# Kernel tuning notes

Hardware: AMD Instinct MI355X
Metric: run time of the kernel (lower is better)

Reference implementation:

```python
import jax, jax.numpy as jnp
import numpy as np

B, S, D, H, NL, FE = 2, 1024, 1024, 16, 6, 4
HD = D // H
DFF = D * FE
EPS = 1e-5


def setup_inputs() -> dict:
    key = jax.random.key(0)
    ks = jax.random.split(key, 12)
    sd = 0.02
    n = lambda k, sh: (jax.random.normal(k, sh, jnp.float32) * sd)
    return {
        "x": jax.random.normal(ks[0], (B, S, D), jnp.float32),
        "pos": n(ks[1], (1, S, D)),
        "Wq": n(ks[2], (NL, HD, HD)), "bq": jnp.zeros((NL, HD), jnp.float32),
        "Wk": n(ks[3], (NL, HD, HD)), "bk": jnp.zeros((NL, HD), jnp.float32),
        "Wv": n(ks[4], (NL, HD, HD)), "bv": jnp.zeros((NL, HD), jnp.float32),
        "Wfc": n(ks[5], (NL, D, D)), "bfc": jnp.zeros((NL, D), jnp.float32),
        "ln1_w": jnp.ones((NL, D), jnp.float32), "ln1_b": jnp.zeros((NL, D), jnp.float32),
        "ln2_w": jnp.ones((NL, D), jnp.float32), "ln2_b": jnp.zeros((NL, D), jnp.float32),
        "W1": n(ks[6], (NL, D, DFF)), "b1": jnp.zeros((NL, DFF), jnp.float32),
        "W2": n(ks[7], (NL, DFF, D)), "b2": jnp.zeros((NL, D), jnp.float32),
        "lnf_w": jnp.ones((D,), jnp.float32), "lnf_b": jnp.zeros((D,), jnp.float32),
    }


def _ln(z, w, b):
    m = jnp.mean(z, axis=-1, keepdims=True)
    v = jnp.mean(jnp.square(z - m), axis=-1, keepdims=True)
    return (z - m) * jax.lax.rsqrt(v + EPS) * w + b


def reference(x, pos, Wq, bq, Wk, bk, Wv, bv, Wfc, bfc,
              ln1_w, ln1_b, ln2_w, ln2_b, W1, b1, W2, b2, lnf_w, lnf_b):
    Bx, Sx, Dx = x.shape
    causal = jnp.tril(jnp.ones((Sx, Sx), bool))  # [S,S], broadcast over b,h
    y = x + pos[:, :Sx, :]
    scale = 1.0 / jnp.sqrt(jnp.float32(HD))
    for i in range(NL):
        yh = y.reshape(Bx, Sx, H, HD)
        # per-head Linear with weights SHARED across heads (as in source)
        q = yh @ Wq[i] + bq[i]
        k = yh @ Wk[i] + bk[i]
        v = yh @ Wv[i] + bv[i]
        score = jnp.einsum("bqhd,bkhd->bhqk", q, k)
        # masked_fill(-1e20) BEFORE scaling, as in source
        score = jnp.where(causal, score, jnp.float32(-1e20)) * scale
        attn = jax.nn.softmax(score, axis=-1)
        o = jnp.einsum("bhqk,bkhd->bqhd", attn, v).reshape(Bx, Sx, D)
        o = o @ Wfc[i] + bfc[i]
        add = _ln(o + y, ln1_w[i], ln1_b[i])
        ff = jax.nn.gelu(add @ W1[i] + b1[i], approximate=False) @ W2[i] + b2[i]
        y = _ln(ff + add, ln2_w[i], ln2_b[i])
    return _ln(y, lnf_w, lnf_b)
```

## Files before the change

kernel.cpp:

```cpp
#include <hip/hip_runtime.h>
#include <hip/hip_bf16.h>
#include <math.h>

#define B_   2
#define S_   1024
#define D_   1024
#define H_   16
#define HD_  64
#define NL_  6
#define DFF_ 4096

typedef __bf16 bf16_t;
typedef bf16_t bf16x8 __attribute__((ext_vector_type(8)));
typedef bf16_t bf16x4 __attribute__((ext_vector_type(4)));
typedef float  f32x4  __attribute__((ext_vector_type(4)));

__device__ __forceinline__ float gelu_exact(float x) {
    return 0.5f * x * (1.0f + erff(x * 0.70710678118654752f));
}

__device__ __forceinline__ void gload16(const bf16_t* g, bf16_t* l) {
    __builtin_amdgcn_global_load_lds(
        (const __attribute__((address_space(1))) void*)g,
        (__attribute__((address_space(3))) void*)l, 16, 0, 0);
}

__global__ __launch_bounds__(256) void add_pos_kernel(
    const float* __restrict__ x, const float* __restrict__ pos,
    float* __restrict__ y, bf16_t* __restrict__ yb)
{
    int idx = blockIdx.x * 256 + threadIdx.x;
    f32x4 xv = *(const f32x4*)&x[idx * 4];
    f32x4 pv = *(const f32x4*)&pos[(idx & 262143) * 4];
    f32x4 o = xv + pv;
    *(f32x4*)&y[idx * 4] = o;
    *(bf16x4*)&yb[idx * 4] = __builtin_convertvector(o, bf16x4);
}

__global__ __launch_bounds__(256) void qkv_mfma_kernel(
    const bf16_t* __restrict__ yb,
    const float* __restrict__ Wq, const float* __restrict__ bq,
    const float* __restrict__ Wk, const float* __restrict__ bk,
    const float* __restrict__ Wv, const float* __restrict__ bv,
    bf16_t* __restrict__ q, bf16_t* __restrict__ k, bf16_t* __restrict__ v)
{
    __shared__ __align__(16) bf16_t As[128][72];
    __shared__ __align__(16) bf16_t Wt[3][64][72];

    int tid = threadIdx.x;
    long m0 = (long)blockIdx.x * 128;

#pragma unroll
    for (int it = 0; it < 4; ++it) {
        int c = it * 256 + tid;
        int row = c >> 3, col = (c & 7) * 8;
        *(bf16x8*)&As[row][col] = *(const bf16x8*)&yb[(m0 + row) * 64 + col];
    }
#pragma unroll
    for (int it = 0; it < 16; ++it) {
        int i = it * 256 + tid;
        int r = i >> 6, c = i & 63;
        Wt[0][c][r] = (bf16_t)Wq[i];
        Wt[1][c][r] = (bf16_t)Wk[i];
        Wt[2][c][r] = (bf16_t)Wv[i];
    }
    __syncthreads();

    int wave = tid >> 6, lane = tid & 63;
    int quad = lane >> 4, l16 = lane & 15;
    int wm = wave * 32;

    bf16x8 a[2][2];
#pragma unroll
    for (int i = 0; i < 2; ++i)
#pragma unroll
        for (int ks = 0; ks < 2; ++ks)
            a[i][ks] = *(bf16x8*)&As[wm + i * 16 + l16][ks * 32 + quad * 8];

    f32x4 acc[3][2][4];
#pragma unroll
    for (int o = 0; o < 3; ++o)
#pragma unroll
        for (int i = 0; i < 2; ++i)
#pragma unroll
            for (int j = 0; j < 4; ++j) acc[o][i][j] = (f32x4)0.f;

#pragma unroll
    for (int o = 0; o < 3; ++o)
#pragma unroll
        for (int j = 0; j < 4; ++j) {
            bf16x8 b0 = *(bf16x8*)&Wt[o][j * 16 + l16][quad * 8];
            bf16x8 b1 = *(bf16x8*)&Wt[o][j * 16 + l16][32 + quad * 8];
#pragma unroll
            for (int i = 0; i < 2; ++i) {
                acc[o][i][j] = __builtin_amdgcn_mfma_f32_16x16x32_bf16(a[i][0], b0, acc[o][i][j], 0, 0, 0);
                acc[o][i][j] = __builtin_amdgcn_mfma_f32_16x16x32_bf16(a[i][1], b1, acc[o][i][j], 0, 0, 0);
            }
        }

    bf16_t* outs[3] = { q, k, v };
    const float* biases[3] = { bq, bk, bv };
#pragma unroll
    for (int o = 0; o < 3; ++o)
#pragma unroll
        for (int j = 0; j < 4; ++j) {
            int col = j * 16 + l16;
            float bias = biases[o][col];
#pragma unroll
            for (int i = 0; i < 2; ++i) {
                long rbase = m0 + wm + i * 16 + quad * 4;
#pragma unroll
                for (int r = 0; r < 4; ++r)
                    outs[o][(rbase + r) * 64 + col] = (bf16_t)(acc[o][i][j][r] + bias);
            }
        }
}

__global__ __launch_bounds__(256) void vtrans_kernel(
    const bf16_t* __restrict__ vb, bf16_t* __restrict__ vT)
{
    __shared__ __align__(16) bf16_t L[32][72];
    int tid = threadIdx.x;
    int s0 = blockIdx.x * 32;
    int bh = blockIdx.y;
    int b = bh >> 4, h = bh & 15;
    int sr = tid >> 3, dc = (tid & 7) * 8;
    *(bf16x8*)&L[sr][dc] =
        *(const bf16x8*)&vb[(((long)b * S_ + s0 + sr) * H_ + h) * HD_ + dc];
    __syncthreads();
    int dr = tid >> 2, sg = (tid & 3) * 8;
    bf16x8 o;
#pragma unroll
    for (int j = 0; j < 8; ++j) o[j] = L[sg + j][dr];
    *(bf16x8*)&vT[((long)bh * HD_ + dr) * S_ + s0 + sg] = o;
}

__global__ __launch_bounds__(256) void attn_mfma_kernel(
    const bf16_t* __restrict__ Q, const bf16_t* __restrict__ K,
    const bf16_t* __restrict__ VT, bf16_t* __restrict__ Ob)
{
    __shared__ __align__(16) bf16_t Ks[64][72];
    __shared__ __align__(16) bf16_t Vt[64][72];
    __shared__ __align__(16) bf16_t Ps[4][16][72];

    int tid = threadIdx.x;
    int wave = tid >> 6, lane = tid & 63;
    int quad = lane >> 4, l16 = lane & 15;
    int qidx = (blockIdx.x < 8) ? (int)blockIdx.x : 23 - (int)blockIdx.x;
    int q0 = qidx * 64;
    int bh = blockIdx.y;
    int b = bh >> 4, h = bh & 15;
    int qw = q0 + wave * 16;
    const float scale = 0.125f;
    const float MASKED = -1.25e19f;

    const bf16_t* Qbase = Q + (((long)b * S_ + qw + l16) * H_ + h) * HD_;
    bf16x8 aq0 = *(const bf16x8*)&Qbase[quad * 8];
    bf16x8 aq1 = *(const bf16x8*)&Qbase[32 + quad * 8];

    float mrun = -3.0e38f, lrun = 0.f;
    f32x4 oacc[4];
#pragma unroll
    for (int n = 0; n < 4; ++n) oacc[n] = (f32x4)0.f;

    int srow = tid >> 3, scol = (tid & 7) * 8;
    const bf16_t* VTbase = VT + ((long)bh * HD_ ) * S_;
    int qg = qw + l16;

    int nkt = qidx + 1;
    for (int kt = 0; kt < nkt; ++kt) {
        int k0 = kt * 64;
        __syncthreads();
#pragma unroll
        for (int half = 0; half < 2; ++half) {
            int row = half * 32 + srow;
            *(bf16x8*)&Ks[row][scol] =
                *(const bf16x8*)&K[(((long)b * S_ + k0 + row) * H_ + h) * HD_ + scol];
            *(bf16x8*)&Vt[row][scol] =
                *(const bf16x8*)&VTbase[(long)row * S_ + k0 + scol];
        }
        __syncthreads();

        if (k0 > qw + 15) continue;

        f32x4 sc[4];
#pragma unroll
        for (int n = 0; n < 4; ++n) sc[n] = (f32x4)0.f;
#pragma unroll
        for (int n = 0; n < 4; ++n) {
            bf16x8 ak0 = *(bf16x8*)&Ks[n * 16 + l16][quad * 8];
            bf16x8 ak1 = *(bf16x8*)&Ks[n * 16 + l16][32 + quad * 8];
            sc[n] = __builtin_amdgcn_mfma_f32_16x16x32_bf16(ak0, aq0, sc[n], 0, 0, 0);
            sc[n] = __builtin_amdgcn_mfma_f32_16x16x32_bf16(ak1, aq1, sc[n], 0, 0, 0);
        }
        float pmax = MASKED;
#pragma unroll
        for (int n = 0; n < 4; ++n)
#pragma unroll
            for (int r = 0; r < 4; ++r) {
                int kv = k0 + n * 16 + quad * 4 + r;
                float sv = (kv <= qg) ? sc[n][r] * scale : MASKED;
                sc[n][r] = sv;
                pmax = fmaxf(pmax, sv);
            }
        pmax = fmaxf(pmax, __shfl_xor(pmax, 16));
        pmax = fmaxf(pmax, __shfl_xor(pmax, 32));
        float mnew = fmaxf(mrun, pmax);
        float ls = 0.f;
#pragma unroll
        for (int n = 0; n < 4; ++n)
#pragma unroll
            for (int r = 0; r < 4; ++r) {
                float pv = __expf(sc[n][r] - mnew);
                sc[n][r] = pv;
                ls += pv;
            }
        ls += __shfl_xor(ls, 16);
        ls += __shfl_xor(ls, 32);
        float alpha = __expf(mrun - mnew);
        lrun = lrun * alpha + ls;
        mrun = mnew;

#pragma unroll
        for (int n = 0; n < 4; ++n)
            *(bf16x4*)&Ps[wave][l16][n * 16 + quad * 4] =
                __builtin_convertvector(sc[n], bf16x4);

        f32x4 av;
#pragma unroll
        for (int r = 0; r < 4; ++r) av[r] = __shfl(alpha, quad * 4 + r);

        bf16x8 pa0 = *(bf16x8*)&Ps[wave][l16][quad * 8];
        bf16x8 pa1 = *(bf16x8*)&Ps[wave][l16][32 + quad * 8];
#pragma unroll
        for (int n = 0; n < 4; ++n) {
            bf16x8 bv0 = *(bf16x8*)&Vt[n * 16 + l16][quad * 8];
            bf16x8 bv1 = *(bf16x8*)&Vt[n * 16 + l16][32 + quad * 8];
            f32x4 c = oacc[n] * av;
            c = __builtin_amdgcn_mfma_f32_16x16x32_bf16(pa0, bv0, c, 0, 0, 0);
            oacc[n] = __builtin_amdgcn_mfma_f32_16x16x32_bf16(pa1, bv1, c, 0, 0, 0);
        }
    }

    float inv = 1.0f / lrun;
    f32x4 iv;
#pragma unroll
    for (int r = 0; r < 4; ++r) iv[r] = __shfl(inv, quad * 4 + r);
#pragma unroll
    for (int r = 0; r < 4; ++r) {
        long rowbase = (((long)b * S_ + qw + quad * 4 + r) * H_ + h) * HD_;
#pragma unroll
        for (int n = 0; n < 4; ++n)
            Ob[rowbase + n * 16 + l16] = (bf16_t)(oacc[n][r] * iv[r]);
    }
}

__global__ __launch_bounds__(256) void tconv_all_kernel(
    const float* __restrict__ Wfc, const float* __restrict__ W1,
    const float* __restrict__ W2, bf16_t* __restrict__ WTall)
{
    int id = blockIdx.x;
    int layer = id / 4608;
    int r = id - layer * 4608;
    const float* W; bf16_t* Wt; int Kd, Nd, tix;
    if (r < 512)       { W = Wfc + (size_t)layer * 1048576; Wt = WTall + (size_t)layer * 9437184;           Kd = 1024; Nd = 1024; tix = r; }
    else if (r < 2560) { W = W1  + (size_t)layer * 4194304; Wt = WTall + (size_t)layer * 9437184 + 1048576; Kd = 1024; Nd = 4096; tix = r - 512; }
    else               { W = W2  + (size_t)layer * 4194304; Wt = WTall + (size_t)layer * 9437184 + 5242880; Kd = 4096; Nd = 1024; tix = r - 2560; }
    int ntx = Nd >> 5;
    int by = tix / ntx, bx = tix - by * ntx;

    __shared__ float t[64][33];
    int tid = threadIdx.x;
    int tx = tid & 31, ty = tid >> 5;
#pragma unroll
    for (int i = 0; i < 8; ++i)
        t[ty + i * 8][tx] = W[(size_t)(by * 64 + ty + i * 8) * Nd + bx * 32 + tx];
    __syncthreads();
    int c = tid >> 3, rg = (tid & 7) * 8;
    bf16x8 o;
#pragma unroll
    for (int j = 0; j < 8; ++j) o[j] = (bf16_t)t[rg + j][c];
    *(bf16x8*)&Wt[(size_t)(bx * 32 + c) * Kd + by * 64 + rg] = o;
}

__global__ __launch_bounds__(256) void gemm_bt_kernel(
    const bf16_t* __restrict__ A, const bf16_t* __restrict__ Bt,
    const float* __restrict__ bias, float* __restrict__ Cf,
    bf16_t* __restrict__ Cb, int M, int N, int K, int act, size_t pstride)
{
    __shared__ __align__(16) bf16_t As[3][128 * 32];
    __shared__ __align__(16) bf16_t Bs[3][64 * 32];
    int tid = threadIdx.x;
    int wave = tid >> 6, lane = tid & 63;
    int quad = lane >> 4, l16 = lane & 15;
    int m0 = blockIdx.x * 128;
    int n0 = blockIdx.y * 64;
    int Kc = K / gridDim.z;
    int kbeg = blockIdx.z * Kc;
    float* Cfp = Cf ? Cf + (size_t)blockIdx.z * pstride : nullptr;

    int wm = (wave >> 1) * 64, wn = (wave & 1) * 32;

    int srow = lane >> 2;
    int sslot = (lane & 3) ^ (srow & 3);
    int rslot = (quad ^ (l16 & 3)) * 8;

    f32x4 acc[4][2];
#pragma unroll
    for (int i = 0; i < 4; ++i)
#pragma unroll
        for (int j = 0; j < 2; ++j) acc[i][j] = (f32x4)0.f;

    const bf16_t* Ab = A + (size_t)(m0 + srow) * K + sslot * 8;
    const bf16_t* Bb = Bt + (size_t)(n0 + wave * 16 + srow) * K + sslot * 8;
    int seg0 = wave * 2;
    int nt = Kc >> 5;

    #define STAGE(t, buf) do {                                                      \
        int kk_ = kbeg + (t) * 32;                                                  \
        gload16(Ab + (size_t)seg0 * 16 * K + kk_, &As[(buf)][seg0 * 512]);          \
        gload16(Ab + (size_t)(seg0 + 1) * 16 * K + kk_, &As[(buf)][(seg0+1) * 512]);\
        gload16(Bb + kk_, &Bs[(buf)][wave * 512]);                                  \
    } while (0)

    #define COMPUTE(buf) do {                                                       \
        bf16x8 af[4], bfr[2];                                                       \
        _Pragma("unroll")                                                           \
        for (int i = 0; i < 4; ++i)                                                 \
            af[i] = *(bf16x8*)&As[(buf)][(wm + i * 16 + l16) * 32 + rslot];         \
        _Pragma("unroll")                                                           \
        for (int j = 0; j < 2; ++j)                                                 \
            bfr[j] = *(bf16x8*)&Bs[(buf)][(wn + j * 16 + l16) * 32 + rslot];        \
        _Pragma("unroll")                                                           \
        for (int i = 0; i < 4; ++i)                                                 \
            _Pragma("unroll")                                                       \
            for (int j = 0; j < 2; ++j)                                             \
                acc[i][j] = __builtin_amdgcn_mfma_f32_16x16x32_bf16(                \
                    af[i], bfr[j], acc[i][j], 0, 0, 0);                             \
    } while (0)

    STAGE(0, 0);
    STAGE(1, 1);

    int cur = 0, pf = 2;
    for (int t = 0; t < nt - 1; ++t) {
        asm volatile("s_waitcnt vmcnt(3)" ::: "memory");
        __builtin_amdgcn_s_barrier();
        __builtin_amdgcn_sched_barrier(0);
        if (t + 2 < nt) STAGE(t + 2, pf);
        COMPUTE(cur);
        cur = (cur == 2) ? 0 : cur + 1;
        pf  = (pf  == 2) ? 0 : pf  + 1;
    }
    asm volatile("s_waitcnt vmcnt(0)" ::: "memory");
    __builtin_amdgcn_s_barrier();
    __builtin_amdgcn_sched_barrier(0);
    COMPUTE(cur);

    #undef STAGE
    #undef COMPUTE

#pragma unroll
    for (int j = 0; j < 2; ++j) {
        int col = n0 + wn + j * 16 + l16;
        float bv = (bias && blockIdx.z == 0) ? bias[col] : 0.f;
#pragma unroll
        for (int i = 0; i < 4; ++i) {
            int rbase = m0 + wm + i * 16 + quad * 4;
#pragma unroll
            for (int r = 0; r < 4; ++r) {
                float vv = acc[i][j][r] + bv;
                if (act == 1) vv = gelu_exact(vv);
                if (Cfp) Cfp[(size_t)(rbase + r) * N + col] = vv;
                if (Cb) Cb[(size_t)(rbase + r) * N + col] = (bf16_t)vv;
            }
        }
    }
}

__global__ __launch_bounds__(256) void ln_fused_kernel(
    const float* __restrict__ a0, const float* __restrict__ a1,
    const float* __restrict__ b,
    const float* __restrict__ w, const float* __restrict__ beta,
    float* __restrict__ out, bf16_t* __restrict__ outb)
{
    long row = blockIdx.x;
    int tid = threadIdx.x;
    f32x4 z = *(const f32x4*)&a0[row * D_ + tid * 4];
    if (a1) z += *(const f32x4*)&a1[row * D_ + tid * 4];
    if (b)  z += *(const f32x4*)&b[row * D_ + tid * 4];
    float s  = z[0] + z[1] + z[2] + z[3];
    float ss = z[0]*z[0] + z[1]*z[1] + z[2]*z[2] + z[3]*z[3];
#pragma unroll
    for (int off = 32; off >= 1; off >>= 1) {
        s  += __shfl_down(s, off);
        ss += __shfl_down(ss, off);
    }
    __shared__ float red[8];
    int lane = tid & 63, wid = tid >> 6;
    if (lane == 0) { red[wid * 2] = s; red[wid * 2 + 1] = ss; }
    __syncthreads();
    s  = red[0] + red[2] + red[4] + red[6];
    ss = red[1] + red[3] + red[5] + red[7];
    float mean = s * (1.0f / D_);
    float var  = ss * (1.0f / D_) - mean * mean;
    float rs = rsqrtf(var + 1e-5f);
    f32x4 wv = *(const f32x4*)&w[tid * 4];
    f32x4 bv = *(const f32x4*)&beta[tid * 4];
    f32x4 o = (z - mean) * rs * wv + bv;
    *(f32x4*)&out[row * D_ + tid * 4] = o;
    if (outb) *(bf16x4*)&outb[row * D_ + tid * 4] = __builtin_convertvector(o, bf16x4);
}

extern "C" void kernel_launch(void* const* d_in, const int* in_sizes, int n_in,
                              void* d_out, int out_size, void* d_ws, size_t ws_size,
                              hipStream_t stream)
{
    (void)in_sizes; (void)n_in; (void)out_size; (void)ws_size;
    const float* x    = (const float*)d_in[0];
    const float* pos  = (const float*)d_in[1];
    const float* Wq   = (const float*)d_in[2];
    const float* bq   = (const float*)d_in[3];
    const float* Wk   = (const float*)d_in[4];
    const float* bk   = (const float*)d_in[5];
    const float* Wv   = (const float*)d_in[6];
    const float* bv   = (const float*)d_in[7];
    const float* Wfc  = (const float*)d_in[8];
    const float* bfc  = (const float*)d_in[9];
    const float* ln1w = (const float*)d_in[10];
    const float* ln1b = (const float*)d_in[11];
    const float* ln2w = (const float*)d_in[12];
    const float* ln2b = (const float*)d_in[13];
    const float* W1   = (const float*)d_in[14];
    const float* b1   = (const float*)d_in[15];
    const float* W2   = (const float*)d_in[16];
    const float* b2   = (const float*)d_in[17];
    const float* lnfw = (const float*)d_in[18];
    const float* lnfb = (const float*)d_in[19];

    const size_t MB = 1 << 20;
    char* ws = (char*)d_ws;
    float*  y    = (float*)(ws);
    bf16_t* yb   = (bf16_t*)(ws + 8 * MB);
    bf16_t* qb   = (bf16_t*)(ws + 12 * MB);
    bf16_t* kb   = (bf16_t*)(ws + 16 * MB);
    bf16_t* vb   = (bf16_t*)(ws + 20 * MB);
    bf16_t* ob   = (bf16_t*)(ws + 24 * MB);
    float*  t1a  = (float*)(ws + 12 * MB);
    float*  t1b  = (float*)(ws + 28 * MB);
    float*  t2a  = (float*)(ws + 12 * MB);
    float*  t2b  = (float*)(ws + 20 * MB);
    float*  add  = (float*)(ws + 28 * MB);
    bf16_t* addb = (bf16_t*)(ws + 36 * MB);
    bf16_t* vTb  = (bf16_t*)(ws + 40 * MB);
    bf16_t* ffb  = (bf16_t*)(ws + 40 * MB);
    bf16_t* WTall= (bf16_t*)(ws + 64 * MB);

    const size_t pstride_wfc  = (size_t)16 * MB / sizeof(float);
    const size_t pstride_ffn2 = (size_t)8 * MB / sizeof(float);
    const size_t LSTRIDE = 9437184;

    tconv_all_kernel<<<27648, 256, 0, stream>>>(Wfc, W1, W2, WTall);

    add_pos_kernel<<<2048, 256, 0, stream>>>(x, pos, y, yb);

    for (int i = 0; i < NL_; ++i) {
        bf16_t* WfcT = WTall + (size_t)i * LSTRIDE;
        bf16_t* W1T  = WfcT + 1048576;
        bf16_t* W2T  = WfcT + 5242880;

        qkv_mfma_kernel<<<256, 256, 0, stream>>>(
            yb, Wq + i * 4096, bq + i * 64, Wk + i * 4096, bk + i * 64,
            Wv + i * 4096, bv + i * 64, qb, kb, vb);

        vtrans_kernel<<<dim3(32, 32), 256, 0, stream>>>(vb, vTb);

        attn_mfma_kernel<<<dim3(16, 32), 256, 0, stream>>>(qb, kb, vTb, ob);

        gemm_bt_kernel<<<dim3(16, 16, 2), 256, 0, stream>>>(
            ob, WfcT, bfc + i * D_, t1a, nullptr, 2048, D_, D_, 0, pstride_wfc);

        ln_fused_kernel<<<2048, 256, 0, stream>>>(
            t1a, t1b, y, ln1w + i * D_, ln1b + i * D_, add, addb);

        gemm_bt_kernel<<<dim3(16, 64, 1), 256, 0, stream>>>(
            addb, W1T, b1 + i * DFF_, nullptr, ffb, 2048, DFF_, D_, 1, 0);

        gemm_bt_kernel<<<dim3(16, 16, 2), 256, 0, stream>>>(
            ffb, W2T, b2 + i * D_, t2a, nullptr, 2048, D_, DFF_, 0, pstride_ffn2);

        ln_fused_kernel<<<2048, 256, 0, stream>>>(
            t2a, t2b, add, ln2w + i * D_, ln2b + i * D_, y, yb);
    }

    ln_fused_kernel<<<2048, 256, 0, stream>>>(
        y, nullptr, nullptr, lnfw, lnfb, (float*)d_out, nullptr);
}
```

Baseline: 1.209 ms.

## Use 128x128 GEMM tiles for FFN and split-K by four for FFN2

Templates the GEMM on the N tile width and adds a 128-wide variant in which each wave computes a 64x64 sub-tile, raising MFMA work per LDS load. FFN1 runs with fewer, larger blocks. FFN2 uses 128-wide tiles with 4-way split-K, and the LayerNorm kernel is extended to sum four partial buffers. The attention kernel's reversed/paired q-block ordering is replaced by plain blockIdx ordering, which may hurt load balance for the causal workload. The larger tiles add register and LDS pressure, and the extra split-K partials add memory traffic.

Measured after the change: 1.188 ms. No clear change (-1.7%).

```diff
diff --git a/kernel.cpp b/kernel.cpp
--- a/kernel.cpp
+++ b/kernel.cpp
@@ -146,8 +146,7 @@
     int tid = threadIdx.x;
     int wave = tid >> 6, lane = tid & 63;
     int quad = lane >> 4, l16 = lane & 15;
-    int qidx = (blockIdx.x < 8) ? (int)blockIdx.x : 23 - (int)blockIdx.x;
-    int q0 = qidx * 64;
+    int q0 = blockIdx.x * 64;
     int bh = blockIdx.y;
     int b = bh >> 4, h = bh & 15;
     int qw = q0 + wave * 16;
@@ -167,7 +166,7 @@
     const bf16_t* VTbase = VT + ((long)bh * HD_ ) * S_;
     int qg = qw + l16;
 
-    int nkt = qidx + 1;
+    int nkt = blockIdx.x + 1;
     for (int kt = 0; kt < nkt; ++kt) {
         int k0 = kt * 64;
         __syncthreads();
@@ -283,36 +282,39 @@
     *(bf16x8*)&Wt[(size_t)(bx * 32 + c) * Kd + by * 64 + rg] = o;
 }
 
+template<int BN>
 __global__ __launch_bounds__(256) void gemm_bt_kernel(
     const bf16_t* __restrict__ A, const bf16_t* __restrict__ Bt,
     const float* __restrict__ bias, float* __restrict__ Cf,
     bf16_t* __restrict__ Cb, int M, int N, int K, int act, size_t pstride)
 {
     __shared__ __align__(16) bf16_t As[3][128 * 32];
-    __shared__ __align__(16) bf16_t Bs[3][64 * 32];
+    __shared__ __align__(16) bf16_t Bs[3][BN * 32];
     int tid = threadIdx.x;
     int wave = tid >> 6, lane = tid & 63;
     int quad = lane >> 4, l16 = lane & 15;
     int m0 = blockIdx.x * 128;
-    int n0 = blockIdx.y * 64;
+    int n0 = blockIdx.y * BN;
     int Kc = K / gridDim.z;
     int kbeg = blockIdx.z * Kc;
     float* Cfp = Cf ? Cf + (size_t)blockIdx.z * pstride : nullptr;
 
-    int wm = (wave >> 1) * 64, wn = (wave & 1) * 32;
+    constexpr int WN = BN / 2;
+    constexpr int NJ = WN / 16;
+    int wm = (wave >> 1) * 64, wn = (wave & 1) * WN;
 
     int srow = lane >> 2;
     int sslot = (lane & 3) ^ (srow & 3);
     int rslot = (quad ^ (l16 & 3)) * 8;
 
-    f32x4 acc[4][2];
+    f32x4 acc[4][NJ];
 #pragma unroll
     for (int i = 0; i < 4; ++i)
 #pragma unroll
-        for (int j = 0; j < 2; ++j) acc[i][j] = (f32x4)0.f;
+        for (int j = 0; j < NJ; ++j) acc[i][j] = (f32x4)0.f;
 
     const bf16_t* Ab = A + (size_t)(m0 + srow) * K + sslot * 8;
-    const bf16_t* Bb = Bt + (size_t)(n0 + wave * 16 + srow) * K + sslot * 8;
+    const bf16_t* Bb = Bt + (size_t)(n0 + srow + (BN == 64 ? wave * 16 : 0)) * K + sslot * 8;
     int seg0 = wave * 2;
     int nt = Kc >> 5;
 
@@ -320,21 +322,26 @@
         int kk_ = kbeg + (t) * 32;                                                  \
         gload16(Ab + (size_t)seg0 * 16 * K + kk_, &As[(buf)][seg0 * 512]);          \
         gload16(Ab + (size_t)(seg0 + 1) * 16 * K + kk_, &As[(buf)][(seg0+1) * 512]);\
-        gload16(Bb + kk_, &Bs[(buf)][wave * 512]);                                  \
+        if constexpr (BN == 64) {                                                   \
+            gload16(Bb + kk_, &Bs[(buf)][wave * 512]);                              \
+        } else {                                                                    \
+            gload16(Bb + (size_t)seg0 * 16 * K + kk_, &Bs[(buf)][seg0 * 512]);      \
+            gload16(Bb + (size_t)(seg0 + 1) * 16 * K + kk_, &Bs[(buf)][(seg0+1) * 512]); \
+        }                                                                           \
     } while (0)
 
     #define COMPUTE(buf) do {                                                       \
-        bf16x8 af[4], bfr[2];                                                       \
+        bf16x8 af[4], bfr[NJ];                                                      \
         _Pragma("unroll")                                                           \
         for (int i = 0; i < 4; ++i)                                                 \
             af[i] = *(bf16x8*)&As[(buf)][(wm + i * 16 + l16) * 32 + rslot];         \
         _Pragma("unroll")                                                           \
-        for (int j = 0; j < 2; ++j)                                                 \
+        for (int j = 0; j < NJ; ++j)                                                \
             bfr[j] = *(bf16x8*)&Bs[(buf)][(wn + j * 16 + l16) * 32 + rslot];        \
         _Pragma("unroll")                                                           \
         for (int i = 0; i < 4; ++i)                                                 \
             _Pragma("unroll")                                                       \
-            for (int j = 0; j < 2; ++j)                                             \
+            for (int j = 0; j < NJ; ++j)                                            \
                 acc[i][j] = __builtin_amdgcn_mfma_f32_16x16x32_bf16(                \
                     af[i], bfr[j], acc[i][j], 0, 0, 0);                             \
     } while (0)
@@ -344,7 +351,8 @@
 
     int cur = 0, pf = 2;
     for (int t = 0; t < nt - 1; ++t) {
-        asm volatile("s_waitcnt vmcnt(3)" ::: "memory");
+        if constexpr (BN == 64) asm volatile("s_waitcnt vmcnt(3)" ::: "memory");
+        else                    asm volatile("s_waitcnt vmcnt(4)" ::: "memory");
         __builtin_amdgcn_s_barrier();
         __builtin_amdgcn_sched_barrier(0);
         if (t + 2 < nt) STAGE(t + 2, pf);
@@ -361,7 +369,7 @@
     #undef COMPUTE
 
 #pragma unroll
-    for (int j = 0; j < 2; ++j) {
+    for (int j = 0; j < NJ; ++j) {
         int col = n0 + wn + j * 16 + l16;
         float bv = (bias && blockIdx.z == 0) ? bias[col] : 0.f;
 #pragma unroll
@@ -380,6 +388,7 @@
 
 __global__ __launch_bounds__(256) void ln_fused_kernel(
     const float* __restrict__ a0, const float* __restrict__ a1,
+    const float* __restrict__ a2, const float* __restrict__ a3,
     const float* __restrict__ b,
     const float* __restrict__ w, const float* __restrict__ beta,
     float* __restrict__ out, bf16_t* __restrict__ outb)
@@ -388,6 +397,8 @@
     int tid = threadIdx.x;
     f32x4 z = *(const f32x4*)&a0[row * D_ + tid * 4];
     if (a1) z += *(const f32x4*)&a1[row * D_ + tid * 4];
+    if (a2) z += *(const f32x4*)&a2[row * D_ + tid * 4];
+    if (a3) z += *(const f32x4*)&a3[row * D_ + tid * 4];
     if (b)  z += *(const f32x4*)&b[row * D_ + tid * 4];
     float s  = z[0] + z[1] + z[2] + z[3];
     float ss = z[0]*z[0] + z[1]*z[1] + z[2]*z[2] + z[3]*z[3];
@@ -448,13 +459,12 @@
     bf16_t* ob   = (bf16_t*)(ws + 24 * MB);
     float*  t1a  = (float*)(ws + 12 * MB);
     float*  t1b  = (float*)(ws + 28 * MB);
-    float*  t2a  = (float*)(ws + 12 * MB);
-    float*  t2b  = (float*)(ws + 20 * MB);
     float*  add  = (float*)(ws + 28 * MB);
     bf16_t* addb = (bf16_t*)(ws + 36 * MB);
     bf16_t* vTb  = (bf16_t*)(ws + 40 * MB);
     bf16_t* ffb  = (bf16_t*)(ws + 40 * MB);
     bf16_t* WTall= (bf16_t*)(ws + 64 * MB);
+    float*  t2p  = (float*)(ws + 172 * MB);
 
     const size_t pstride_wfc  = (size_t)16 * MB / sizeof(float);
     const size_t pstride_ffn2 = (size_t)8 * MB / sizeof(float);
@@ -477,22 +487,23 @@
 
         attn_mfma_kernel<<<dim3(16, 32), 256, 0, stream>>>(qb, kb, vTb, ob);
 
-        gemm_bt_kernel<<<dim3(16, 16, 2), 256, 0, stream>>>(
+        gemm_bt_kernel<64><<<dim3(16, 16, 2), 256, 0, stream>>>(
             ob, WfcT, bfc + i * D_, t1a, nullptr, 2048, D_, D_, 0, pstride_wfc);
 
         ln_fused_kernel<<<2048, 256, 0, stream>>>(
-            t1a, t1b, y, ln1w + i * D_, ln1b + i * D_, add, addb);
-
-        gemm_bt_kernel<<<dim3(16, 64, 1), 256, 0, stream>>>(
+            t1a, t1b, nullptr, nullptr, y, ln1w + i * D_, ln1b + i * D_, add, addb);
+
+        gemm_bt_kernel<128><<<dim3(16, 32, 1), 256, 0, stream>>>(
             addb, W1T, b1 + i * DFF_, nullptr, ffb, 2048, DFF_, D_, 1, 0);
 
-        gemm_bt_kernel<<<dim3(16, 16, 2), 256, 0, stream>>>(
-            ffb, W2T, b2 + i * D_, t2a, nullptr, 2048, D_, DFF_, 0, pstride_ffn2);
+        gemm_bt_kernel<128><<<dim3(16, 8, 4), 256, 0, stream>>>(
+            ffb, W2T, b2 + i * D_, t2p, nullptr, 2048, D_, DFF_, 0, pstride_ffn2);
 
         ln_fused_kernel<<<2048, 256, 0, stream>>>(
-            t2a, t2b, add, ln2w + i * D_, ln2b + i * D_, y, yb);
+            t2p, t2p + pstride_ffn2, t2p + 2 * pstride_ffn2, t2p + 3 * pstride_ffn2,
+            add, ln2w + i * D_, ln2b + i * D_, y, yb);
     }
 
     ln_fused_kernel<<<2048, 256, 0, stream>>>(
-        y, nullptr, nullptr, lnfw, lnfb, (float*)d_out, nullptr);
-}
+        y, nullptr, nullptr, nullptr, nullptr, lnfw, lnfb, (float*)d_out, nullptr);
+}
```
